# Performance work log

Hardware: AMD Instinct MI355X
Metric: run time of the kernel (lower is better)

Reference implementation:

```python
import jax, jax.numpy as jnp
import numpy as np

NUM_EMBEDDINGS = 512
EMBEDDING_DIM = 384
COMMITMENT_BETA = 0.25
N_TOKENS = 262144


def setup_inputs() -> dict:
    key = jax.random.key(0)
    kz, ke = jax.random.split(key)
    z = jax.random.normal(kz, (N_TOKENS, EMBEDDING_DIM), dtype=jnp.float32)
    # nn.init.normal_(weight, mean=0.0, std=0.02)
    emb = 0.02 * jax.random.normal(ke, (NUM_EMBEDDINGS, EMBEDDING_DIM), dtype=jnp.float32)
    return {"z": z, "emb": emb}


def reference(z, emb):
    # Squared L2 distances via norms + matmul (same math as broadcast (z-e)^2 sum,
    # without materializing the [N, K, D] tensor).
    z_sq = jnp.sum(z * z, axis=1, keepdims=True)          # [N, 1]
    e_sq = jnp.sum(emb * emb, axis=1)                     # [K]
    distances = z_sq - 2.0 * (z @ emb.T) + e_sq           # [N, K]
    nearest_idx = jnp.argmin(distances, axis=1)           # [N]
    z_q = emb[nearest_idx]                                # [N, D] gather
    loss_codebook = jnp.mean((z_q - z) ** 2)
    loss_commit = loss_codebook  # same value in fwd; grads differ only in bwd
    vq_loss = loss_codebook + COMMITMENT_BETA * loss_commit
    # straight-through: z + (z_q - z).detach() equals z_q numerically in fwd
    z_q_out = z + jax.lax.stop_gradient(z_q - z)
    return (z_q_out, nearest_idx, vq_loss)
```

## Files before the change

### kernel.cpp

```cpp
#include <hip/hip_runtime.h>
#include <stdint.h>

#define NTOK 262144
#define DIM 384
#define KC 512

constexpr int MT = 64;
constexpr int DC = 16;
constexpr int LST = DC + 4;

__global__ void esq_kernel(const float* __restrict__ emb, float* __restrict__ ws) {
#pragma clang fp contract(off)
    int k = blockIdx.x * blockDim.x + threadIdx.x;
    if (k == 0) *(double*)(ws + 512) = 0.0;
    if (k < KC) {
        const float* e = emb + (size_t)k * DIM;
        float s96[4];
        for (int c = 0; c < 4; ++c) {
            const float* p = e + c * 96;
            float r[8];
#pragma unroll
            for (int j = 0; j < 8; ++j) {
                float q = p[j] * p[j];
                r[j] = q;
            }
            for (int i = 8; i < 96; i += 8) {
#pragma unroll
                for (int j = 0; j < 8; ++j) {
                    float q = p[i + j] * p[i + j];
                    r[j] = r[j] + q;
                }
            }
            s96[c] = ((r[0] + r[1]) + (r[2] + r[3])) + ((r[4] + r[5]) + (r[6] + r[7]));
        }
        ws[k] = (s96[0] + s96[1]) + (s96[2] + s96[3]);
    }
}

__launch_bounds__(256, 2)
__global__ void vq_main(const float* __restrict__ z, const float* __restrict__ emb,
                        const float* __restrict__ ws_esq, double* __restrict__ ws_loss,
                        float* __restrict__ out_zq, float* __restrict__ out_idx) {
    __shared__ float z_lds[MT][LST];
    __shared__ float e_lds[KC][LST];
    __shared__ float esq_lds[KC];
    __shared__ float zsq_part[4][MT];
    __shared__ float zsq_lds[MT];
    __shared__ unsigned long long win_lds[MT];
    __shared__ float loss_part[8];

    const int t   = threadIdx.x;
    const int kid = t & 31;
    const int mid = t >> 5;
    const int m0  = blockIdx.x * MT;

    esq_lds[t]       = ws_esq[t];
    esq_lds[t + 256] = ws_esq[t + 256];

    float acc[8][16];
#pragma unroll
    for (int a = 0; a < 8; ++a)
#pragma unroll
        for (int b = 0; b < 16; ++b) acc[a][b] = 0.f;

    float zsq_p = 0.f;
    const int sr = t >> 2;
    const int sc = (t & 3) << 2;

    for (int dc = 0; dc < DIM; dc += DC) {
        __syncthreads();
        {
            float4 v = *(const float4*)(z + (size_t)(m0 + sr) * DIM + dc + sc);
            *(float4*)&z_lds[sr][sc] = v;
        }
#pragma unroll
        for (int i = 0; i < 8; ++i) {
            int k = sr + (i << 6);
            float4 v = *(const float4*)(emb + (size_t)k * DIM + dc + sc);
            *(float4*)&e_lds[k][sc] = v;
        }
        __syncthreads();
        {
            int m = t & 63, q = t >> 6;
#pragma unroll
            for (int dd = 0; dd < 4; ++dd) {
                float v = z_lds[m][q * 4 + dd];
                zsq_p = fmaf(v, v, zsq_p);
            }
        }
#pragma unroll
        for (int d4 = 0; d4 < DC; d4 += 4) {
            float4 a[8];
#pragma unroll
            for (int mi = 0; mi < 8; ++mi)
                a[mi] = *(const float4*)&z_lds[mid * 8 + mi][d4];
#pragma unroll
            for (int j = 0; j < 16; ++j) {
                float4 b = *(const float4*)&e_lds[kid + (j << 5)][d4];
#pragma unroll
                for (int mi = 0; mi < 8; ++mi) {
                    float s = acc[mi][j];
                    s = fmaf(a[mi].x, b.x, s);
                    s = fmaf(a[mi].y, b.y, s);
                    s = fmaf(a[mi].z, b.z, s);
                    s = fmaf(a[mi].w, b.w, s);
                    acc[mi][j] = s;
                }
            }
        }
    }

    zsq_part[t >> 6][t & 63] = zsq_p;
    __syncthreads();
    if (t < MT)
        zsq_lds[t] = (zsq_part[0][t] + zsq_part[1][t]) + (zsq_part[2][t] + zsq_part[3][t]);
    __syncthreads();

    float row_loss = 0.f;
#pragma unroll
    for (int mi = 0; mi < 8; ++mi) {
        int r = mid * 8 + mi;
        float zs = zsq_lds[r];
        unsigned long long best = ~0ull;
#pragma unroll
        for (int j = 0; j < 16; ++j) {
            int k = kid + (j << 5);
            float t1 = fmaf(-2.f, acc[mi][j], zs);
            float dist = t1 + esq_lds[k];
            unsigned long long p =
                ((unsigned long long)__float_as_uint(dist) << 32) | (unsigned)k;
            best = p < best ? p : best;
        }
#pragma unroll
        for (int off = 16; off > 0; off >>= 1) {
            unsigned long long o = __shfl_xor(best, off);
            best = o < best ? o : best;
        }
        if (kid == 0) {
            win_lds[r] = best;
            out_idx[m0 + r] = (float)(unsigned)(best & 0xffffffffu);
            row_loss += __uint_as_float((unsigned)(best >> 32));
        }
    }
    if (kid == 0) loss_part[mid] = row_loss;
    __syncthreads();
    if (t == 0) {
        float s = 0.f;
        for (int i = 0; i < 8; ++i) s += loss_part[i];
        atomicAdd(ws_loss, (double)s);
    }

#pragma unroll
    for (int p = 0; p < 8; ++p) {
        int r = (p << 3) + mid;
        unsigned idx = (unsigned)(win_lds[r] & 0xffffffffu);
        const float* er = emb + (size_t)idx * DIM;
        float* orow = out_zq + (size_t)(m0 + r) * DIM;
        for (int c = kid * 4; c < DIM; c += 128)
            *(float4*)(orow + c) = *(const float4*)(er + c);
    }
}

__global__ void finalize_kernel(const double* __restrict__ ws_loss, float* __restrict__ out_loss) {
    if (threadIdx.x == 0 && blockIdx.x == 0) {
        double s = *ws_loss;
        *out_loss = (float)(1.25 * s / (double)((size_t)NTOK * DIM));
    }
}

extern "C" void kernel_launch(void* const* d_in, const int* in_sizes, int n_in,
                              void* d_out, int out_size, void* d_ws, size_t ws_size,
                              hipStream_t stream) {
    const float* z   = (const float*)d_in[0];
    const float* emb = (const float*)d_in[1];
    float* out     = (float*)d_out;
    float* ws      = (float*)d_ws;
    float* out_zq  = out;
    float* out_idx = out + (size_t)NTOK * DIM;
    float* out_ls  = out + (size_t)NTOK * DIM + NTOK;

    esq_kernel<<<2, 256, 0, stream>>>(emb, ws);
    vq_main<<<NTOK / MT, 256, 0, stream>>>(z, emb, ws, (double*)(ws + 512), out_zq, out_idx);
    finalize_kernel<<<1, 1, 0, stream>>>((const double*)(ws + 512), out_ls);
}
```

Measured before the change: 1.993 ms.

## Load z and codebook tiles directly to LDS with global_load_lds and new layout

```diff
diff --git a/kernel.cpp b/kernel.cpp
--- a/kernel.cpp
+++ b/kernel.cpp
@@ -6,8 +6,13 @@
 #define KC 512
 
 constexpr int MT = 64;
-constexpr int DC = 16;
-constexpr int LST = DC + 4;
+
+typedef unsigned int u32;
+__device__ __forceinline__ void gload16(const float* g, float* l) {
+    __builtin_amdgcn_global_load_lds(
+        (__attribute__((address_space(1))) u32*)g,
+        (__attribute__((address_space(3))) u32*)l, 16, 0, 0);
+}
 
 __global__ void esq_kernel(const float* __restrict__ emb, float* __restrict__ ws) {
 #pragma clang fp contract(off)
@@ -41,10 +46,9 @@
 __global__ void vq_main(const float* __restrict__ z, const float* __restrict__ emb,
                         const float* __restrict__ ws_esq, double* __restrict__ ws_loss,
                         float* __restrict__ out_zq, float* __restrict__ out_idx) {
-    __shared__ float z_lds[MT][LST];
-    __shared__ float e_lds[KC][LST];
+    __shared__ __align__(16) float z_lds[MT * 16];
+    __shared__ __align__(16) float e_lds[KC * 16];
     __shared__ float esq_lds[KC];
-    __shared__ float zsq_part[4][MT];
     __shared__ float zsq_lds[MT];
     __shared__ unsigned long long win_lds[MT];
     __shared__ float loss_part[8];
@@ -52,6 +56,7 @@
     const int t   = threadIdx.x;
     const int kid = t & 31;
     const int mid = t >> 5;
+    const int wv  = t >> 6;
     const int m0  = blockIdx.x * MT;
 
     esq_lds[t]       = ws_esq[t];
@@ -64,56 +69,56 @@
         for (int b = 0; b < 16; ++b) acc[a][b] = 0.f;
 
     float zsq_p = 0.f;
-    const int sr = t >> 2;
-    const int sc = (t & 3) << 2;
 
-    for (int dc = 0; dc < DIM; dc += DC) {
+    const float* zsrc = z + (size_t)(m0 + (t >> 2)) * DIM + ((t & 3) << 2);
+    float* zdst = z_lds + (wv << 8);
+    const int krow = ((t >> 7) << 5) + kid;
+    const float* esrc = emb + (size_t)krow * DIM + (((t >> 5) & 3) << 2);
+    float* edst = e_lds + (wv << 8);
+
+    for (int dc = 0; dc < DIM; dc += 16) {
         __syncthreads();
+        gload16(zsrc + dc, zdst);
+#pragma unroll
+        for (int i = 0; i < 8; ++i)
+            gload16(esrc + dc + i * (64 * DIM), edst + (i << 10));
+        __syncthreads();
+
         {
-            float4 v = *(const float4*)(z + (size_t)(m0 + sr) * DIM + dc + sc);
-            *(float4*)&z_lds[sr][sc] = v;
+            float4 v = *((const float4*)z_lds + t);
+            zsq_p = fmaf(v.x, v.x, zsq_p);
+            zsq_p = fmaf(v.y, v.y, zsq_p);
+            zsq_p = fmaf(v.z, v.z, zsq_p);
+            zsq_p = fmaf(v.w, v.w, zsq_p);
         }
+
+        const float4* z4 = (const float4*)z_lds;
+        const float4* e4 = (const float4*)e_lds;
 #pragma unroll
-        for (int i = 0; i < 8; ++i) {
-            int k = sr + (i << 6);
-            float4 v = *(const float4*)(emb + (size_t)k * DIM + dc + sc);
-            *(float4*)&e_lds[k][sc] = v;
-        }
-        __syncthreads();
-        {
-            int m = t & 63, q = t >> 6;
-#pragma unroll
-            for (int dd = 0; dd < 4; ++dd) {
-                float v = z_lds[m][q * 4 + dd];
-                zsq_p = fmaf(v, v, zsq_p);
-            }
-        }
-#pragma unroll
-        for (int d4 = 0; d4 < DC; d4 += 4) {
+        for (int s = 0; s < 4; ++s) {
             float4 a[8];
 #pragma unroll
             for (int mi = 0; mi < 8; ++mi)
-                a[mi] = *(const float4*)&z_lds[mid * 8 + mi][d4];
+                a[mi] = z4[(((mid << 3) + mi) << 2) + s];
 #pragma unroll
             for (int j = 0; j < 16; ++j) {
-                float4 b = *(const float4*)&e_lds[kid + (j << 5)][d4];
+                float4 b = e4[(j << 7) + (s << 5) + kid];
 #pragma unroll
                 for (int mi = 0; mi < 8; ++mi) {
-                    float s = acc[mi][j];
-                    s = fmaf(a[mi].x, b.x, s);
-                    s = fmaf(a[mi].y, b.y, s);
-                    s = fmaf(a[mi].z, b.z, s);
-                    s = fmaf(a[mi].w, b.w, s);
-                    acc[mi][j] = s;
+                    float sum = acc[mi][j];
+                    sum = fmaf(a[mi].x, b.x, sum);
+                    sum = fmaf(a[mi].y, b.y, sum);
+                    sum = fmaf(a[mi].z, b.z, sum);
+                    sum = fmaf(a[mi].w, b.w, sum);
+                    acc[mi][j] = sum;
                 }
             }
         }
     }
 
-    zsq_part[t >> 6][t & 63] = zsq_p;
-    __syncthreads();
-    if (t < MT)
-        zsq_lds[t] = (zsq_part[0][t] + zsq_part[1][t]) + (zsq_part[2][t] + zsq_part[3][t]);
+    zsq_p += __shfl_xor(zsq_p, 1);
+    zsq_p += __shfl_xor(zsq_p, 2);
+    if ((t & 3) == 0) zsq_lds[t >> 2] = zsq_p;
     __syncthreads();
 
     float row_loss = 0.f;
```

Result: slower. 5.711 ms (+186.6%).
